# Performance work log

Hardware: AMD Instinct MI355X
Metric: run time of the kernel (lower is better)

The kernel has to match this reference:

```python
import jax, jax.numpy as jnp
import numpy as np

EMBED_DIM = 1024
NUM_HEADS = 16
HEAD_DIM = EMBED_DIM // NUM_HEADS


def setup_inputs() -> dict:
    key = jax.random.key(0)
    ks = jax.random.split(key, 11)
    B, S, D = 2, 2048, EMBED_DIM
    s = 1.0 / np.sqrt(D)
    inp = {
        "q": jax.random.normal(ks[0], (B, S, D), jnp.float32),
        "k": jax.random.normal(ks[1], (B, S, D), jnp.float32),
        "v": jax.random.normal(ks[2], (B, S, D), jnp.float32),
        # Linear params stored as (in, out) so y = x @ W + b
        "wq": jax.random.uniform(ks[3], (D, D), jnp.float32, -s, s),
        "bq": jax.random.uniform(ks[4], (D,), jnp.float32, -s, s),
        "wk": jax.random.uniform(ks[5], (D, D), jnp.float32, -s, s),
        "bk": jax.random.uniform(ks[6], (D,), jnp.float32, -s, s),
        "wv": jax.random.uniform(ks[7], (D, D), jnp.float32, -s, s),
        "bv": jax.random.uniform(ks[8], (D,), jnp.float32, -s, s),
        "wo": jax.random.uniform(ks[9], (D, D), jnp.float32, -s, s),
        "bo": jax.random.uniform(ks[10], (D,), jnp.float32, -s, s),
    }
    return inp


def reference(q, k, v, wq, bq, wk, bk, wv, bv, wo, bo):
    B, S, D = q.shape
    H, Hd = NUM_HEADS, HEAD_DIM
    temperature = Hd ** 0.5

    def proj(x, w, b):
        # (B, S, D) -> (B, H, S, Hd)
        y = x @ w + b
        return y.reshape(B, S, H, Hd).transpose(0, 2, 1, 3)

    qh = proj(q, wq, bq)
    kh = proj(k, wk, bk)
    vh = proj(v, wv, bv)

    # naive attention with materialized [B, H, S, S] scores (faithful to source)
    scores = jnp.einsum("bhqd,bhkd->bhqk", qh / temperature, kh)
    attn = jax.nn.softmax(scores, axis=-1)
    ctx = jnp.einsum("bhqk,bhkd->bhqd", attn, vh)

    ctx = ctx.transpose(0, 2, 1, 3).reshape(B, S, D)
    out = ctx @ wo + bo
    return out, attn
```

## Files before the change

### kernel.cpp

```cpp
#include <hip/hip_runtime.h>

#define S_   2048
#define D_   1024

typedef __attribute__((ext_vector_type(8))) __bf16 bf16x8;
typedef __attribute__((ext_vector_type(4))) __bf16 bf16x4;
typedef __attribute__((ext_vector_type(4))) float f32x4;
typedef __attribute__((ext_vector_type(4))) float float4v;
typedef __attribute__((ext_vector_type(2))) unsigned int u32x2;
typedef __attribute__((ext_vector_type(4))) unsigned int u32x4;

#define XQ_OFF   0
#define XK_OFF   4194304
#define XV_OFF   8388608
#define WQT_OFF  12582912
#define WKT_OFF  13631488
#define WVT_OFF  14680064
#define WOT_OFF  15728640
#define QH_OFF   16777216
#define KH_OFF   20971520
#define VHT_OFF  25165824
#define CTX_OFF  29360128
#define WS_BYTES 67108864ULL

#if __has_builtin(__builtin_amdgcn_exp2f)
#define EXP2(x) __builtin_amdgcn_exp2f(x)
#else
#define EXP2(x) __expf((x) * 0.69314718056f)
#endif
#define QSCALE 0.1803368801f

__device__ __forceinline__ unsigned short f2b(float f) {
  unsigned u = __builtin_bit_cast(unsigned, f);
  u += 0x7fffu + ((u >> 16) & 1u);
  return (unsigned short)(u >> 16);
}
__device__ __forceinline__ float b2f(unsigned s) {
  return __builtin_bit_cast(float, s << 16);
}

__global__ __launch_bounds__(256) void cvt_qkv(const float* __restrict__ q,
    const float* __restrict__ k, const float* __restrict__ v,
    short* __restrict__ ws) {
  const float* src = (blockIdx.y == 0) ? q : (blockIdx.y == 1) ? k : v;
  short* dst = ws + (size_t)blockIdx.y * 4194304;
  size_t t = (size_t)blockIdx.x * 256 + threadIdx.x;
  float4v f = *(const float4v*)(src + t * 4);
  u32x2 p;
  p[0] = (unsigned)f2b(f[0]) | ((unsigned)f2b(f[1]) << 16);
  p[1] = (unsigned)f2b(f[2]) | ((unsigned)f2b(f[3]) << 16);
  *(u32x2*)(dst + t * 4) = p;
}

__global__ __launch_bounds__(256) void cvt_wt(const float* __restrict__ wq,
    const float* __restrict__ wk, const float* __restrict__ wv,
    const float* __restrict__ wo, short* __restrict__ ws) {
  __shared__ float tile[32][33];
  int z = blockIdx.z;
  const float* W = (z == 0) ? wq : (z == 1) ? wk : (z == 2) ? wv : wo;
  short* Wt = ws + WQT_OFF + (size_t)z * 1048576;
  int tx = threadIdx.x, ty = threadIdx.y;
#pragma unroll
  for (int i = 0; i < 4; ++i)
    tile[ty + i * 8][tx] =
        W[(size_t)(blockIdx.y * 32 + ty + i * 8) * D_ + blockIdx.x * 32 + tx];
  __syncthreads();
#pragma unroll
  for (int i = 0; i < 4; ++i)
    Wt[(size_t)(blockIdx.x * 32 + ty + i * 8) * D_ + blockIdx.y * 32 + tx] =
        (short)f2b(tile[tx][ty + i * 8]);
}

__device__ __forceinline__ void stage_tile(const short* __restrict__ g,
                                           short* l, int w, int lane) {
  int lrow = lane >> 3, lcol = (lane & 7) * 8;
#pragma unroll
  for (int c = 0; c < 4; ++c) {
    int seg = c * 4 + w;
    const short* gp = g + (size_t)(seg * 8 + lrow) * 1024 + lcol;
    short* lp = l + seg * 512 + lane * 8;
    __builtin_amdgcn_global_load_lds(
        (const __attribute__((address_space(1))) void*)gp,
        (__attribute__((address_space(3))) void*)lp, 16, 0, 0);
  }
}

__global__ __launch_bounds__(256) void gemm_bf16(short* __restrict__ ws,
    const float* __restrict__ bq, const float* __restrict__ bk,
    const float* __restrict__ bv, const float* __restrict__ bo,
    float* __restrict__ out, int mode_base) {
  const int tid = threadIdx.x, lane = tid & 63, w = tid >> 6;
  const int wm = w >> 1, wn = w & 1;
  const int ln15 = lane & 15, g = lane >> 4;
  const int bm = blockIdx.y, bn = blockIdx.x;
  const int mode = (mode_base == 3) ? 3 : (int)blockIdx.z;

  const short* A; const short* Bt; const float* bias;
  if (mode == 0)      { A = ws + XQ_OFF;  Bt = ws + WQT_OFF; bias = bq; }
  else if (mode == 1) { A = ws + XK_OFF;  Bt = ws + WKT_OFF; bias = bk; }
  else if (mode == 2) { A = ws + XV_OFF;  Bt = ws + WVT_OFF; bias = bv; }
  else                { A = ws + CTX_OFF; Bt = ws + WOT_OFF; bias = bo; }

  __shared__ short smem[2][2][8192];
  short (*sA)[8192] = smem[0];
  short (*sB)[8192] = smem[1];

  f32x4 acc[4][4] = {};

  const short* Ab = A + (size_t)bm * 128 * 1024;
  const short* Bb = Bt + (size_t)bn * 128 * 1024;

  stage_tile(Ab, sA[0], w, lane);
  stage_tile(Bb, sB[0], w, lane);
  __syncthreads();

  int cur = 0;
#pragma unroll 1
  for (int kt = 0; kt < 16; ++kt) {
    if (kt < 15) {
      stage_tile(Ab + (kt + 1) * 64, sA[cur ^ 1], w, lane);
      stage_tile(Bb + (kt + 1) * 64, sB[cur ^ 1], w, lane);
    }
#pragma unroll
    for (int kk = 0; kk < 2; ++kk) {
      bf16x8 af[4], bfr[4];
#pragma unroll
      for (int m = 0; m < 4; ++m)
        af[m] = *(const bf16x8*)&sA[cur][(wm * 64 + m * 16 + ln15) * 64 + kk * 32 + g * 8];
#pragma unroll
      for (int n = 0; n < 4; ++n)
        bfr[n] = *(const bf16x8*)&sB[cur][(wn * 64 + n * 16 + ln15) * 64 + kk * 32 + g * 8];
#pragma unroll
      for (int m = 0; m < 4; ++m)
#pragma unroll
        for (int n = 0; n < 4; ++n)
          acc[m][n] = __builtin_amdgcn_mfma_f32_16x16x32_bf16(af[m], bfr[n], acc[m][n], 0, 0, 0);
    }
    __syncthreads();
    cur ^= 1;
  }

  float bb[4];
#pragma unroll
  for (int n = 0; n < 4; ++n) bb[n] = bias[bn * 128 + wn * 64 + n * 16 + ln15];

  if (mode == 3) {
#pragma unroll
    for (int m = 0; m < 4; ++m) {
      int row0 = bm * 128 + wm * 64 + m * 16 + g * 4;
#pragma unroll
      for (int n = 0; n < 4; ++n) {
        int col = bn * 128 + wn * 64 + n * 16 + ln15;
#pragma unroll
        for (int r = 0; r < 4; ++r)
          out[(size_t)(row0 + r) * 1024 + col] = acc[m][n][r] + bb[n];
      }
    }
    return;
  }

  float sc = (mode == 0) ? QSCALE : 1.0f;
  short (*tile)[136] = (short(*)[136])smem;
#pragma unroll
  for (int m = 0; m < 4; ++m)
#pragma unroll
    for (int n = 0; n < 4; ++n)
#pragma unroll
      for (int r = 0; r < 4; ++r)
        tile[wm * 64 + m * 16 + g * 4 + r][wn * 64 + n * 16 + ln15] =
            (short)f2b((acc[m][n][r] + bb[n]) * sc);
  __syncthreads();

  if (mode == 2) {
    int dcol = tid >> 1, sh = (tid & 1) * 64;
    int colg = bn * 128 + dcol, h = colg >> 6, hd = colg & 63;
    int b = bm >> 4, sblk = bm & 15;
    short* dst = ws + VHT_OFF +
                 ((size_t)((b * 16 + h) * 16 + sblk)) * 8192 + hd * 128 + sh;
#pragma unroll
    for (int j = 0; j < 8; ++j) {
      u32x4 pk;
#pragma unroll
      for (int q = 0; q < 4; ++q) {
        unsigned lo = (unsigned short)tile[sh + j * 8 + q * 2][dcol];
        unsigned hi = (unsigned short)tile[sh + j * 8 + q * 2 + 1][dcol];
        pk[q] = lo | (hi << 16);
      }
      *(u32x4*)(dst + j * 8) = pk;
    }
  } else {
    int r = tid >> 1, sh = (tid & 1) * 64;
    int colg = bn * 128 + sh, h = colg >> 6;
    int sg = bm * 128 + r, b = sg >> 11, sl = sg & 2047;
    short* dst = ws + ((mode == 0) ? QH_OFF : KH_OFF) +
                 (((size_t)(b * 16 + h)) * 2048 + sl) * 64;
#pragma unroll
    for (int j = 0; j < 8; ++j)
      *(u32x4*)(dst + j * 8) = *(const u32x4*)&tile[r][sh + j * 8];
  }
}

__global__ __launch_bounds__(512) void attn_k(short* __restrict__ ws,
                                              float* __restrict__ attn) {
  const int tid = threadIdx.x, lane = tid & 63, w = tid >> 6;
  const int ln15 = lane & 15, g = lane >> 4;
  int bid = blockIdx.x;
  int qt = (bid >> 3) & 15;
  int bh = (bid & 7) + 8 * (bid >> 7);
  const int q0 = qt * 128;

  const short* Q  = ws + QH_OFF  + ((size_t)bh * 2048 + q0) * 64;
  const short* K  = ws + KH_OFF  + (size_t)bh * 2048 * 64;
  const short* Vt = ws + VHT_OFF + (size_t)bh * 131072;

  __shared__ short sK[2][4096];
  __shared__ short sV[2][4096];
  __shared__ short Pl[128][72];

  const int srow = tid >> 3, sc = tid & 7;
  const int scsw = sc ^ (srow & 7);
  const int sdst = tid * 8;

#define STAGE_K(kt, buf)                                                     \
  __builtin_amdgcn_global_load_lds(                                         \
      (const __attribute__((address_space(1))) void*)(K + ((kt) * 64 + srow) * 64 + scsw * 8), \
      (__attribute__((address_space(3))) void*)(&sK[buf][sdst]), 16, 0, 0)
#define STAGE_V(kt, buf)                                                     \
  __builtin_amdgcn_global_load_lds(                                         \
      (const __attribute__((address_space(1))) void*)(Vt + ((kt) >> 1) * 8192 + srow * 128 + ((kt) & 1) * 64 + scsw * 8), \
      (__attribute__((address_space(3))) void*)(&sV[buf][sdst]), 16, 0, 0)

  bf16x8 qf0 = *(const bf16x8*)&Q[(w * 16 + ln15) * 64 + g * 8];
  bf16x8 qf1 = *(const bf16x8*)&Q[(w * 16 + ln15) * 64 + 32 + g * 8];

  STAGE_K(0, 0);
  asm volatile("s_waitcnt vmcnt(0)" ::: "memory");
  __builtin_amdgcn_s_barrier();

  float ps0 = 0.f, ps1 = 0.f;
  int cur = 0;
#pragma unroll 1
  for (int kt = 0; kt < 32; ++kt) {
    if (kt < 31) STAGE_K(kt + 1, cur ^ 1);
#pragma unroll
    for (int m = 0; m < 4; ++m) {
      int r = m * 16 + ln15;
      bf16x8 ka0 = *(const bf16x8*)&sK[cur][r * 64 + ((g ^ (r & 7)) * 8)];
      bf16x8 ka1 = *(const bf16x8*)&sK[cur][r * 64 + (((4 + g) ^ (r & 7)) * 8)];
      f32x4 c = {0.f, 0.f, 0.f, 0.f};
      c = __builtin_amdgcn_mfma_f32_16x16x32_bf16(ka0, qf0, c, 0, 0, 0);
      c = __builtin_amdgcn_mfma_f32_16x16x32_bf16(ka1, qf1, c, 0, 0, 0);
      ps0 += EXP2(c[0]) + EXP2(c[1]);
      ps1 += EXP2(c[2]) + EXP2(c[3]);
    }
    asm volatile("s_waitcnt vmcnt(0)" ::: "memory");
    __builtin_amdgcn_s_barrier();
    cur ^= 1;
  }
  float ps = ps0 + ps1;
  ps += __shfl_xor(ps, 16, 64);
  ps += __shfl_xor(ps, 32, 64);
  float ri = 1.0f / ps;

  STAGE_K(0, 0);
  STAGE_V(0, 0);
  asm volatile("s_waitcnt vmcnt(0)" ::: "memory");
  __builtin_amdgcn_s_barrier();

  f32x4 cacc[4] = {};
  cur = 0;
#pragma unroll 1
  for (int kt = 0; kt < 32; ++kt) {
    if (kt < 31) {
      STAGE_K(kt + 1, cur ^ 1);
      STAGE_V(kt + 1, cur ^ 1);
    }
#pragma unroll
    for (int m = 0; m < 4; ++m) {
      int r = m * 16 + ln15;
      bf16x8 ka0 = *(const bf16x8*)&sK[cur][r * 64 + ((g ^ (r & 7)) * 8)];
      bf16x8 ka1 = *(const bf16x8*)&sK[cur][r * 64 + (((4 + g) ^ (r & 7)) * 8)];
      f32x4 c = {0.f, 0.f, 0.f, 0.f};
      c = __builtin_amdgcn_mfma_f32_16x16x32_bf16(ka0, qf0, c, 0, 0, 0);
      c = __builtin_amdgcn_mfma_f32_16x16x32_bf16(ka1, qf1, c, 0, 0, 0);
      bf16x4 pb;
      pb[0] = (__bf16)(EXP2(c[0]) * ri);
      pb[1] = (__bf16)(EXP2(c[1]) * ri);
      pb[2] = (__bf16)(EXP2(c[2]) * ri);
      pb[3] = (__bf16)(EXP2(c[3]) * ri);
      *(bf16x4*)&Pl[w * 16 + ln15][m * 16 + g * 4] = pb;
    }
    asm volatile("s_waitcnt lgkmcnt(0)" ::: "memory");
    __builtin_amdgcn_sched_barrier(0);

#pragma unroll
    for (int kk = 0; kk < 2; ++kk) {
      bf16x8 pa = *(const bf16x8*)&Pl[w * 16 + ln15][kk * 32 + g * 8];
#pragma unroll
      for (int n = 0; n < 4; ++n) {
        int vr = n * 16 + ln15;
        bf16x8 vb =
            *(const bf16x8*)&sV[cur][vr * 64 + (((kk * 4 + g) ^ (vr & 7)) * 8)];
        cacc[n] = __builtin_amdgcn_mfma_f32_16x16x32_bf16(pa, vb, cacc[n], 0, 0, 0);
      }
    }

    float* ab = attn + ((size_t)(bh * 2048 + q0 + w * 16)) * 2048 + kt * 64 + lane;
#pragma unroll
    for (int r = 0; r < 16; ++r) {
      unsigned short u = (unsigned short)Pl[w * 16 + r][lane];
      ab[(size_t)r * 2048] = b2f(u);
    }

    asm volatile("s_waitcnt vmcnt(16)" ::: "memory");
    __builtin_amdgcn_s_barrier();
    cur ^= 1;
  }

  {
    short* Pw = &Pl[w * 16][0];
#pragma unroll
    for (int n = 0; n < 4; ++n)
#pragma unroll
      for (int r = 0; r < 4; ++r)
        Pw[(g * 4 + r) * 72 + n * 16 + ln15] = (short)f2b(cacc[n][r]);
    asm volatile("s_waitcnt lgkmcnt(0)" ::: "memory");
    __builtin_amdgcn_sched_barrier(0);
    int b = bh >> 4, h = bh & 15;
    int row = lane >> 3, col = (lane & 7) * 8;
#pragma unroll
    for (int i = 0; i < 2; ++i) {
      int q = q0 + w * 16 + i * 8 + row;
      u32x4 pk = *(const u32x4*)&Pw[(i * 8 + row) * 72 + col];
      *(u32x4*)&ws[CTX_OFF + ((size_t)(b * 2048 + q)) * 1024 + h * 64 + col] = pk;
    }
  }
#undef STAGE_K
#undef STAGE_V
}

extern "C" void kernel_launch(void* const* d_in, const int* in_sizes, int n_in,
                              void* d_out, int out_size, void* d_ws, size_t ws_size,
                              hipStream_t stream) {
  const float* q  = (const float*)d_in[0];
  const float* k  = (const float*)d_in[1];
  const float* v  = (const float*)d_in[2];
  const float* wq = (const float*)d_in[3];
  const float* bq = (const float*)d_in[4];
  const float* wk = (const float*)d_in[5];
  const float* bk = (const float*)d_in[6];
  const float* wv = (const float*)d_in[7];
  const float* bv = (const float*)d_in[8];
  const float* wo = (const float*)d_in[9];
  const float* bo = (const float*)d_in[10];
  float* out  = (float*)d_out;
  float* attn = out + 4194304;
  short* ws = (short*)d_ws;
  if (ws_size < WS_BYTES) return;

  cvt_qkv<<<dim3(4096, 3), 256, 0, stream>>>(q, k, v, ws);
  cvt_wt<<<dim3(32, 32, 4), dim3(32, 8), 0, stream>>>(wq, wk, wv, wo, ws);
  gemm_bf16<<<dim3(8, 32, 3), 256, 0, stream>>>(ws, bq, bk, bv, bo, out, 0);
  attn_k<<<dim3(512), 512, 0, stream>>>(ws, attn);
  gemm_bf16<<<dim3(8, 32, 1), 256, 0, stream>>>(ws, bq, bk, bv, bo, out, 3);
}
```

Measured before the change: 268.9 us.

## Software-pipeline attention P computation with PV and merge conversion kernels

The attention kernel's second pass is software-pipelined. QK^T, exp and the P write for tile i+1 go into a double-buffered P tile (PlA/PlB) while the PV MFMAs and attn stores for tile i run, with K prefetched two tiles ahead. The first pass (row-sum) now stages 128 keys per iteration to halve its barrier count. The two input-conversion kernels are merged into one launch to save a launch. This adds LDS usage (four KV buffers plus two P tiles) and more complex wait and barrier ordering, which could lower occupancy or add hazard risk.

```diff
diff --git a/kernel.cpp b/kernel.cpp
--- a/kernel.cpp
+++ b/kernel.cpp
@@ -39,35 +39,39 @@
   return __builtin_bit_cast(float, s << 16);
 }
 
-__global__ __launch_bounds__(256) void cvt_qkv(const float* __restrict__ q,
+__global__ __launch_bounds__(256) void cvt_all(const float* __restrict__ q,
     const float* __restrict__ k, const float* __restrict__ v,
+    const float* __restrict__ wq, const float* __restrict__ wk,
+    const float* __restrict__ wv, const float* __restrict__ wo,
     short* __restrict__ ws) {
-  const float* src = (blockIdx.y == 0) ? q : (blockIdx.y == 1) ? k : v;
-  short* dst = ws + (size_t)blockIdx.y * 4194304;
-  size_t t = (size_t)blockIdx.x * 256 + threadIdx.x;
-  float4v f = *(const float4v*)(src + t * 4);
-  u32x2 p;
-  p[0] = (unsigned)f2b(f[0]) | ((unsigned)f2b(f[1]) << 16);
-  p[1] = (unsigned)f2b(f[2]) | ((unsigned)f2b(f[3]) << 16);
-  *(u32x2*)(dst + t * 4) = p;
-}
-
-__global__ __launch_bounds__(256) void cvt_wt(const float* __restrict__ wq,
-    const float* __restrict__ wk, const float* __restrict__ wv,
-    const float* __restrict__ wo, short* __restrict__ ws) {
   __shared__ float tile[32][33];
-  int z = blockIdx.z;
+  int b = blockIdx.x, tid = threadIdx.x;
+  if (b < 12288) {
+    int y = b >> 12, x = b & 4095;
+    const float* src = (y == 0) ? q : (y == 1) ? k : v;
+    short* dst = ws + (size_t)y * 4194304;
+    size_t t = (size_t)x * 256 + tid;
+    float4v f = *(const float4v*)(src + t * 4);
+    u32x2 p;
+    p[0] = (unsigned)f2b(f[0]) | ((unsigned)f2b(f[1]) << 16);
+    p[1] = (unsigned)f2b(f[2]) | ((unsigned)f2b(f[3]) << 16);
+    *(u32x2*)(dst + t * 4) = p;
+    return;
+  }
+  int b2 = b - 12288;
+  int z = b2 >> 10, rem = b2 & 1023;
+  int by = rem >> 5, bx = rem & 31;
   const float* W = (z == 0) ? wq : (z == 1) ? wk : (z == 2) ? wv : wo;
   short* Wt = ws + WQT_OFF + (size_t)z * 1048576;
-  int tx = threadIdx.x, ty = threadIdx.y;
+  int tx = tid & 31, ty = tid >> 5;
 #pragma unroll
   for (int i = 0; i < 4; ++i)
     tile[ty + i * 8][tx] =
-        W[(size_t)(blockIdx.y * 32 + ty + i * 8) * D_ + blockIdx.x * 32 + tx];
+        W[(size_t)(by * 32 + ty + i * 8) * D_ + bx * 32 + tx];
   __syncthreads();
 #pragma unroll
   for (int i = 0; i < 4; ++i)
-    Wt[(size_t)(blockIdx.x * 32 + ty + i * 8) * D_ + blockIdx.y * 32 + tx] =
+    Wt[(size_t)(bx * 32 + ty + i * 8) * D_ + by * 32 + tx] =
         (short)f2b(tile[tx][ty + i * 8]);
 }
 
@@ -203,7 +207,7 @@
 __global__ __launch_bounds__(512) void attn_k(short* __restrict__ ws,
                                               float* __restrict__ attn) {
   const int tid = threadIdx.x, lane = tid & 63, w = tid >> 6;
-  const int ln15 = lane & 15, g = lane >> 4;
+  const int ln15 = lane & 15, g = lane >> 4, ln7 = lane & 7;
   int bid = blockIdx.x;
   int qt = (bid >> 3) & 15;
   int bh = (bid & 7) + 8 * (bid >> 7);
@@ -213,40 +217,49 @@
   const short* K  = ws + KH_OFF  + (size_t)bh * 2048 * 64;
   const short* Vt = ws + VHT_OFF + (size_t)bh * 131072;
 
-  __shared__ short sK[2][4096];
-  __shared__ short sV[2][4096];
-  __shared__ short Pl[128][72];
+  __shared__ short sKV[4][4096];
+  __shared__ short PlA[128][72];
+  __shared__ short PlB[128][72];
 
   const int srow = tid >> 3, sc = tid & 7;
   const int scsw = sc ^ (srow & 7);
   const int sdst = tid * 8;
 
-#define STAGE_K(kt, buf)                                                     \
-  __builtin_amdgcn_global_load_lds(                                         \
-      (const __attribute__((address_space(1))) void*)(K + ((kt) * 64 + srow) * 64 + scsw * 8), \
-      (__attribute__((address_space(3))) void*)(&sK[buf][sdst]), 16, 0, 0)
-#define STAGE_V(kt, buf)                                                     \
-  __builtin_amdgcn_global_load_lds(                                         \
+#define STAGE1(t1, b)                                                         \
+  do {                                                                        \
+    __builtin_amdgcn_global_load_lds(                                         \
+        (const __attribute__((address_space(1))) void*)(K + ((t1) * 128 + srow) * 64 + scsw * 8),      \
+        (__attribute__((address_space(3))) void*)(&sKV[2 * (b)][sdst]), 16, 0, 0);                     \
+    __builtin_amdgcn_global_load_lds(                                         \
+        (const __attribute__((address_space(1))) void*)(K + ((t1) * 128 + 64 + srow) * 64 + scsw * 8), \
+        (__attribute__((address_space(3))) void*)(&sKV[2 * (b) + 1][sdst]), 16, 0, 0);                 \
+  } while (0)
+#define STAGE_K2(kt)                                                          \
+  __builtin_amdgcn_global_load_lds(                                           \
+      (const __attribute__((address_space(1))) void*)(K + ((kt) * 64 + srow) * 64 + scsw * 8),         \
+      (__attribute__((address_space(3))) void*)(&sKV[(kt) & 1][sdst]), 16, 0, 0)
+#define STAGE_V2(kt)                                                          \
+  __builtin_amdgcn_global_load_lds(                                           \
       (const __attribute__((address_space(1))) void*)(Vt + ((kt) >> 1) * 8192 + srow * 128 + ((kt) & 1) * 64 + scsw * 8), \
-      (__attribute__((address_space(3))) void*)(&sV[buf][sdst]), 16, 0, 0)
+      (__attribute__((address_space(3))) void*)(&sKV[2 + ((kt) & 1)][sdst]), 16, 0, 0)
 
   bf16x8 qf0 = *(const bf16x8*)&Q[(w * 16 + ln15) * 64 + g * 8];
   bf16x8 qf1 = *(const bf16x8*)&Q[(w * 16 + ln15) * 64 + 32 + g * 8];
 
-  STAGE_K(0, 0);
+  STAGE1(0, 0);
   asm volatile("s_waitcnt vmcnt(0)" ::: "memory");
   __builtin_amdgcn_s_barrier();
 
   float ps0 = 0.f, ps1 = 0.f;
-  int cur = 0;
 #pragma unroll 1
-  for (int kt = 0; kt < 32; ++kt) {
-    if (kt < 31) STAGE_K(kt + 1, cur ^ 1);
-#pragma unroll
-    for (int m = 0; m < 4; ++m) {
-      int r = m * 16 + ln15;
-      bf16x8 ka0 = *(const bf16x8*)&sK[cur][r * 64 + ((g ^ (r & 7)) * 8)];
-      bf16x8 ka1 = *(const bf16x8*)&sK[cur][r * 64 + (((4 + g) ^ (r & 7)) * 8)];
+  for (int t = 0; t < 16; ++t) {
+    int b = t & 1;
+    if (t < 15) STAGE1(t + 1, b ^ 1);
+#pragma unroll
+    for (int m = 0; m < 8; ++m) {
+      const short* kbase = &sKV[2 * b + (m >> 2)][((m * 16 + ln15) & 63) * 64];
+      bf16x8 ka0 = *(const bf16x8*)&kbase[(g ^ ln7) * 8];
+      bf16x8 ka1 = *(const bf16x8*)&kbase[((4 + g) ^ ln7) * 8];
       f32x4 c = {0.f, 0.f, 0.f, 0.f};
       c = __builtin_amdgcn_mfma_f32_16x16x32_bf16(ka0, qf0, c, 0, 0, 0);
       c = __builtin_amdgcn_mfma_f32_16x16x32_bf16(ka1, qf1, c, 0, 0, 0);
@@ -255,70 +268,71 @@
     }
     asm volatile("s_waitcnt vmcnt(0)" ::: "memory");
     __builtin_amdgcn_s_barrier();
-    cur ^= 1;
   }
   float ps = ps0 + ps1;
   ps += __shfl_xor(ps, 16, 64);
   ps += __shfl_xor(ps, 32, 64);
   float ri = 1.0f / ps;
 
-  STAGE_K(0, 0);
-  STAGE_V(0, 0);
+#define QKT_BODY(kti, PLW)                                                    \
+  do {                                                                        \
+    _Pragma("unroll") for (int m = 0; m < 4; ++m) {                           \
+      const short* kbase = &sKV[(kti) & 1][(m * 16 + ln15) * 64];             \
+      bf16x8 ka0 = *(const bf16x8*)&kbase[(g ^ ln7) * 8];                     \
+      bf16x8 ka1 = *(const bf16x8*)&kbase[((4 + g) ^ ln7) * 8];               \
+      f32x4 c = {0.f, 0.f, 0.f, 0.f};                                         \
+      c = __builtin_amdgcn_mfma_f32_16x16x32_bf16(ka0, qf0, c, 0, 0, 0);      \
+      c = __builtin_amdgcn_mfma_f32_16x16x32_bf16(ka1, qf1, c, 0, 0, 0);      \
+      bf16x4 pb;                                                              \
+      pb[0] = (__bf16)(EXP2(c[0]) * ri);                                      \
+      pb[1] = (__bf16)(EXP2(c[1]) * ri);                                      \
+      pb[2] = (__bf16)(EXP2(c[2]) * ri);                                      \
+      pb[3] = (__bf16)(EXP2(c[3]) * ri);                                      \
+      *(bf16x4*)&PLW[w * 16 + ln15][m * 16 + g * 4] = pb;                     \
+    }                                                                         \
+  } while (0)
+
+#define FULL_BODY(i, PLR, PLW)                                                \
+  do {                                                                        \
+    if ((i) < 30) STAGE_K2((i) + 2);                                          \
+    if ((i) < 31) STAGE_V2((i) + 1);                                          \
+    if ((i) < 31) QKT_BODY((i) + 1, PLW);                                     \
+    _Pragma("unroll") for (int kk = 0; kk < 2; ++kk) {                        \
+      bf16x8 pa = *(const bf16x8*)&PLR[w * 16 + ln15][kk * 32 + g * 8];       \
+      _Pragma("unroll") for (int n = 0; n < 4; ++n) {                         \
+        const short* vbase = &sKV[2 + ((i) & 1)][(n * 16 + ln15) * 64];       \
+        bf16x8 vb = *(const bf16x8*)&vbase[((kk * 4 + g) ^ ln7) * 8];         \
+        cacc[n] = __builtin_amdgcn_mfma_f32_16x16x32_bf16(pa, vb, cacc[n], 0, 0, 0); \
+      }                                                                       \
+    }                                                                         \
+    {                                                                         \
+      float* ab = attn + ((size_t)(bh * 2048 + q0 + w * 16)) * 2048 + (i) * 64 + lane; \
+      _Pragma("unroll") for (int r = 0; r < 16; ++r)                          \
+        ab[(size_t)r * 2048] = b2f((unsigned short)PLR[w * 16 + r][lane]);    \
+    }                                                                         \
+    asm volatile("s_waitcnt vmcnt(16)" ::: "memory");                         \
+    __builtin_amdgcn_s_barrier();                                             \
+  } while (0)
+
+  f32x4 cacc[4] = {};
+
+  STAGE_K2(0);
+  STAGE_V2(0);
+  STAGE_K2(1);
   asm volatile("s_waitcnt vmcnt(0)" ::: "memory");
   __builtin_amdgcn_s_barrier();
-
-  f32x4 cacc[4] = {};
-  cur = 0;
+  QKT_BODY(0, PlA);
+  asm volatile("s_waitcnt lgkmcnt(0)" ::: "memory");
+  __builtin_amdgcn_s_barrier();
+
 #pragma unroll 1
-  for (int kt = 0; kt < 32; ++kt) {
-    if (kt < 31) {
-      STAGE_K(kt + 1, cur ^ 1);
-      STAGE_V(kt + 1, cur ^ 1);
-    }
-#pragma unroll
-    for (int m = 0; m < 4; ++m) {
-      int r = m * 16 + ln15;
-      bf16x8 ka0 = *(const bf16x8*)&sK[cur][r * 64 + ((g ^ (r & 7)) * 8)];
-      bf16x8 ka1 = *(const bf16x8*)&sK[cur][r * 64 + (((4 + g) ^ (r & 7)) * 8)];
-      f32x4 c = {0.f, 0.f, 0.f, 0.f};
-      c = __builtin_amdgcn_mfma_f32_16x16x32_bf16(ka0, qf0, c, 0, 0, 0);
-      c = __builtin_amdgcn_mfma_f32_16x16x32_bf16(ka1, qf1, c, 0, 0, 0);
-      bf16x4 pb;
-      pb[0] = (__bf16)(EXP2(c[0]) * ri);
-      pb[1] = (__bf16)(EXP2(c[1]) * ri);
-      pb[2] = (__bf16)(EXP2(c[2]) * ri);
-      pb[3] = (__bf16)(EXP2(c[3]) * ri);
-      *(bf16x4*)&Pl[w * 16 + ln15][m * 16 + g * 4] = pb;
-    }
-    asm volatile("s_waitcnt lgkmcnt(0)" ::: "memory");
-    __builtin_amdgcn_sched_barrier(0);
-
-#pragma unroll
-    for (int kk = 0; kk < 2; ++kk) {
-      bf16x8 pa = *(const bf16x8*)&Pl[w * 16 + ln15][kk * 32 + g * 8];
-#pragma unroll
-      for (int n = 0; n < 4; ++n) {
-        int vr = n * 16 + ln15;
-        bf16x8 vb =
-            *(const bf16x8*)&sV[cur][vr * 64 + (((kk * 4 + g) ^ (vr & 7)) * 8)];
-        cacc[n] = __builtin_amdgcn_mfma_f32_16x16x32_bf16(pa, vb, cacc[n], 0, 0, 0);
-      }
-    }
-
-    float* ab = attn + ((size_t)(bh * 2048 + q0 + w * 16)) * 2048 + kt * 64 + lane;
-#pragma unroll
-    for (int r = 0; r < 16; ++r) {
-      unsigned short u = (unsigned short)Pl[w * 16 + r][lane];
-      ab[(size_t)r * 2048] = b2f(u);
-    }
-
-    asm volatile("s_waitcnt vmcnt(16)" ::: "memory");
-    __builtin_amdgcn_s_barrier();
-    cur ^= 1;
+  for (int i2 = 0; i2 < 32; i2 += 2) {
+    FULL_BODY(i2, PlA, PlB);
+    FULL_BODY(i2 + 1, PlB, PlA);
   }
 
   {
-    short* Pw = &Pl[w * 16][0];
+    short* Pw = &PlA[w * 16][0];
 #pragma unroll
     for (int n = 0; n < 4; ++n)
 #pragma unroll
@@ -335,8 +349,11 @@
       *(u32x4*)&ws[CTX_OFF + ((size_t)(b * 2048 + q)) * 1024 + h * 64 + col] = pk;
     }
   }
-#undef STAGE_K
-#undef STAGE_V
+#undef STAGE1
+#undef STAGE_K2
+#undef STAGE_V2
+#undef QKT_BODY
+#undef FULL_BODY
 }
 
 extern "C" void kernel_launch(void* const* d_in, const int* in_sizes, int n_in,
@@ -358,8 +375,7 @@
   short* ws = (short*)d_ws;
   if (ws_size < WS_BYTES) return;
 
-  cvt_qkv<<<dim3(4096, 3), 256, 0, stream>>>(q, k, v, ws);
-  cvt_wt<<<dim3(32, 32, 4), dim3(32, 8), 0, stream>>>(wq, wk, wv, wo, ws);
+  cvt_all<<<dim3(16384), 256, 0, stream>>>(q, k, v, wq, wk, wv, wo, ws);
   gemm_bf16<<<dim3(8, 32, 3), 256, 0, stream>>>(ws, bq, bk, bv, bo, out, 0);
   attn_k<<<dim3(512), 512, 0, stream>>>(ws, attn);
   gemm_bf16<<<dim3(8, 32, 1), 256, 0, stream>>>(ws, bq, bk, bv, bo, out, 3);
```

Result: no change. 271.8 us (+1.1%).
